# Performance work log

Measured on AMD Instinct MI355X. Metric: run time of the kernel, lower is better.

The kernel has to match this reference:

```python
import jax, jax.numpy as jnp
import numpy as np

MAX_DISP = 40  # search range -> D = 2*MAX_DISP+1 = 81 cost channels
STRIDE = 1


def setup_inputs() -> dict:
    key = jax.random.key(0)
    k1, k2 = jax.random.split(key)
    B, C, H, W = 4, 256, 128, 416
    left = jax.random.normal(k1, (B, C, H, W), dtype=jnp.float32)
    right = jax.random.normal(k2, (B, C, H, W), dtype=jnp.float32)
    return {"left": left, "right": right}


def reference(left, right):
    # mode='time', reduction='mean': per horizontal shift i, cost = mean_C(left * shift(right, i))
    B, C, H, W = left.shape
    rp = jnp.pad(right, ((0, 0), (0, 0), (0, 0), (MAX_DISP, MAX_DISP)))  # [B,C,H,W+2M]
    costs = []
    for i in range(-MAX_DISP, MAX_DISP + 1, STRIDE):  # fixed small unrolled loop over 81 shifts
        sl = jax.lax.dynamic_slice_in_dim(rp, i + MAX_DISP, W, axis=3)  # [B,C,H,W]
        costs.append(jnp.mean(left * sl, axis=1, keepdims=True))        # [B,1,H,W]
    return jnp.concatenate(costs, axis=1)  # [B, 81, H, W]
```

## Files before the change

### kernel.cpp

```cpp
#include <hip/hip_runtime.h>
#include <hip/hip_bf16.h>
#include <stdint.h>

typedef __bf16 bf16x8 __attribute__((ext_vector_type(8)));
typedef float f32x4 __attribute__((ext_vector_type(4)));

#define MAXD 40
#define ND   81
#define CSZ  256
#define HSZ  128
#define WSZ  416
#define HW   (HSZ * WSZ)

#define ALC  448
#define EL   0
#define ER   7168
#define OL   14336
#define ORR  21504
#define ESTR 420

union U8 { uint32_t u[4]; bf16x8 v; };

static __device__ __forceinline__ uint32_t pk2(float a, float b) {
    union { __bf16 h[2]; uint32_t u; } v;
    v.h[0] = (__bf16)a; v.h[1] = (__bf16)b;
    return v.u;
}

static __device__ __forceinline__ void gl16(const float* g, const float* l) {
    __builtin_amdgcn_global_load_lds(
        (const __attribute__((address_space(1))) void*)(uintptr_t)g,
        (__attribute__((address_space(3))) void*)(uint32_t)(uintptr_t)l,
        16, 0, 0);
}

static __device__ __forceinline__ void full_barrier() {
    asm volatile("s_waitcnt vmcnt(0) lgkmcnt(0)" ::: "memory");
    __builtin_amdgcn_s_barrier();
    __builtin_amdgcn_sched_barrier(0);
}

__global__ __launch_bounds__(1024)
void corr_mfma_kernel(const float* __restrict__ left,
                      const float* __restrict__ right,
                      float* __restrict__ out) {
    __shared__ float Sh[28672];

    const int t   = threadIdx.x;
    const int wv  = t >> 6;
    const int l   = t & 63;
    const int l15 = l & 15;
    const int l4  = l >> 4;
    const int b   = blockIdx.x >> 7;
    const int h   = blockIdx.x & 127;

    const size_t slab = ((size_t)b * CSZ) * HW + (size_t)h * WSZ;
    const float* gLw = left  + slab + (size_t)wv * HW + 4 * l;
    const float* gRw = right + slab + (size_t)wv * HW + 4 * l;
    const int shw = 8 * ((wv >> 2) & 3);
    const float* dEL = &Sh[EL  + wv * ALC + shw];
    const float* dER = &Sh[ER  + wv * ALC + shw];
    const float* dOL = &Sh[OL  + wv * ALC + shw];
    const float* dOR = &Sh[ORR + wv * ALC + shw];

    const int p0 = 2 * wv;
    const bool hasP1 = (wv < 15);
    int  cb[2]; bool okb[2];
    #pragma unroll
    for (int pi = 0; pi < 2; ++pi) {
        const int u = 16 * (p0 + pi) - MAXD + l15;
        okb[pi] = ((unsigned)u < (unsigned)WSZ);
        cb[pi]  = okb[pi] ? u : 0;
    }
    const int FB = 1800 * l4;

    f32x4 acc0[6], acc1[6];
    #pragma unroll
    for (int k = 0; k < 6; ++k) { acc0[k] = (f32x4)0.0f; acc1[k] = (f32x4)0.0f; }

    {
        gl16(gLw, dEL); gl16(gRw, dER);
        if (l < 40) { gl16(gLw + 256, dEL + 256); gl16(gRw + 256, dER + 256); }
    }
    full_barrier();

    for (int m = 0; m < 8; ++m) {
        {
            const size_t co = (size_t)(2 * m + 1) * 16 * HW;
            gl16(gLw + co, dOL); gl16(gRw + co, dOR);
            if (l < 40) { gl16(gLw + co + 256, dOL + 256); gl16(gRw + co + 256, dOR + 256); }
        }
        uint2 aLo[7], bLo[2];
        #pragma unroll
        for (int pi = 0; pi < 2; ++pi) {
            if (pi == 0 || hasP1) {
                float v0 = Sh[ER + FB +   0 + cb[pi]];
                float v1 = Sh[ER + FB + 448 + cb[pi]];
                float v2 = Sh[ER + FB + 896 + cb[pi]];
                float v3 = Sh[ER + FB + 1344 + cb[pi]];
                if (!okb[pi]) { v0 = v1 = v2 = v3 = 0.0f; }
                bLo[pi] = make_uint2(pk2(v0, v1), pk2(v2, v3));
            } else bLo[pi] = make_uint2(0u, 0u);
        }
        #pragma unroll
        for (int a = 0; a < 7; ++a) {
            const int r = p0 - 5 + a;
            if (r >= 0 && r <= 25) {
                const int col = 16 * r + l15;
                const float v0 = Sh[EL + FB +   0 + col];
                const float v1 = Sh[EL + FB + 448 + col];
                const float v2 = Sh[EL + FB + 896 + col];
                const float v3 = Sh[EL + FB + 1344 + col];
                aLo[a] = make_uint2(pk2(v0, v1), pk2(v2, v3));
            } else aLo[a] = make_uint2(0u, 0u);
        }
        full_barrier();

        if (m < 7) {
            const size_t co = (size_t)(2 * m + 2) * 16 * HW;
            gl16(gLw + co, dEL); gl16(gRw + co, dER);
            if (l < 40) { gl16(gLw + co + 256, dEL + 256); gl16(gRw + co + 256, dER + 256); }
        }
        bf16x8 bF[2];
        #pragma unroll
        for (int pi = 0; pi < 2; ++pi) {
            if (pi == 0 || hasP1) {
                float v0 = Sh[ORR + FB +   0 + cb[pi]];
                float v1 = Sh[ORR + FB + 448 + cb[pi]];
                float v2 = Sh[ORR + FB + 896 + cb[pi]];
                float v3 = Sh[ORR + FB + 1344 + cb[pi]];
                if (!okb[pi]) { v0 = v1 = v2 = v3 = 0.0f; }
                U8 x; x.u[0] = bLo[pi].x; x.u[1] = bLo[pi].y;
                x.u[2] = pk2(v0, v1); x.u[3] = pk2(v2, v3);
                bF[pi] = x.v;
            }
        }
        #pragma unroll
        for (int a = 0; a < 7; ++a) {
            const int r = p0 - 5 + a;
            if (r >= 0 && r <= 25) {
                const int col = 16 * r + l15;
                const float v0 = Sh[OL + FB +   0 + col];
                const float v1 = Sh[OL + FB + 448 + col];
                const float v2 = Sh[OL + FB + 896 + col];
                const float v3 = Sh[OL + FB + 1344 + col];
                U8 x; x.u[0] = aLo[a].x; x.u[1] = aLo[a].y;
                x.u[2] = pk2(v0, v1); x.u[3] = pk2(v2, v3);
                if (a < 6)
                    acc0[a] = __builtin_amdgcn_mfma_f32_16x16x32_bf16(x.v, bF[0], acc0[a], 0, 0, 0);
                if (hasP1 && a >= 1)
                    acc1[a - 1] = __builtin_amdgcn_mfma_f32_16x16x32_bf16(x.v, bF[1], acc1[a - 1], 0, 0, 0);
            }
        }
        full_barrier();
    }

    const float scale = 1.0f / 256.0f;
    float* outp = out + (size_t)b * ND * HW + (size_t)h * WSZ;

    #pragma unroll
    for (int gph = 0; gph < 2; ++gph) {
        const int d0 = gph * 41;
        const int dn = gph ? 40 : 41;

        #pragma unroll
        for (int pi = 0; pi < 2; ++pi) {
            if (pi == 0 || hasP1) {
                #pragma unroll
                for (int k = 0; k < 6; ++k) {
                    const int r = p0 - 5 + pi + k;
                    if (r >= 0 && r <= 25) {
                        const int j = 5 - k;
                        const f32x4 av = pi ? acc1[k] : acc0[k];
                        #pragma unroll
                        for (int rr = 0; rr < 4; ++rr) {
                            const int mm = 4 * l4 + rr;
                            const int d  = 16 * j + l15 - mm;
                            if ((unsigned)(d - d0) < (unsigned)dn)
                                Sh[(d - d0) * ESTR + 16 * r + mm] = av[rr] * scale;
                        }
                    }
                }
            }
        }
        full_barrier();

        #pragma unroll
        for (int i = 0; i < 5; ++i) {
            const int idx = i * 1024 + t;
            if (idx < dn * 104) {
                const int d = idx / 104;
                const int q = idx - 104 * d;
                *(f32x4*)(outp + (size_t)(d0 + d) * HW + 4 * q) = *(const f32x4*)&Sh[d * ESTR + 4 * q];
            }
        }
        if (gph == 0) full_barrier();
    }
}

extern "C" void kernel_launch(void* const* d_in, const int* in_sizes, int n_in,
                              void* d_out, int out_size, void* d_ws, size_t ws_size,
                              hipStream_t stream) {
    const float* left  = (const float*)d_in[0];
    const float* right = (const float*)d_in[1];
    float* out = (float*)d_out;
    (void)in_sizes; (void)n_in; (void)out_size; (void)d_ws; (void)ws_size;
    corr_mfma_kernel<<<dim3(4 * 128), dim3(1024), 0, stream>>>(left, right, out);
}
```

Before: 101.6 us.

## Triple-buffer LDS channel chunks with prefetch depth two and partial vmcnt waits

Replaces the even/odd double buffer with a three-slot LDS ring, so each 16-channel chunk is prefetched two steps ahead. Barriers wait with vmcnt(4) instead of draining all outstanding global loads, which lets the next chunk's loads stay in flight during compute. The padded row stride and swizzle offset are dropped to fit three buffers, which risks more LDS bank conflicts and grows shared memory to about 160KB.

New measurement: 105.7 us. +4.1%, slower.

```diff
diff --git a/kernel.cpp b/kernel.cpp
--- a/kernel.cpp
+++ b/kernel.cpp
@@ -12,12 +12,11 @@
 #define WSZ  416
 #define HW   (HSZ * WSZ)
 
-#define ALC  448
-#define EL   0
-#define ER   7168
-#define OL   14336
-#define ORR  21504
-#define ESTR 420
+#define ALC   420
+#define RHALF 6720
+#define BUFD  13440
+#define NCHK  16
+#define ESTR  420
 
 union U8 { uint32_t u[4]; bf16x8 v; };
 
@@ -34,17 +33,11 @@
         16, 0, 0);
 }
 
-static __device__ __forceinline__ void full_barrier() {
-    asm volatile("s_waitcnt vmcnt(0) lgkmcnt(0)" ::: "memory");
-    __builtin_amdgcn_s_barrier();
-    __builtin_amdgcn_sched_barrier(0);
-}
-
 __global__ __launch_bounds__(1024)
 void corr_mfma_kernel(const float* __restrict__ left,
                       const float* __restrict__ right,
                       float* __restrict__ out) {
-    __shared__ float Sh[28672];
+    __shared__ float Sh[3 * BUFD];
 
     const int t   = threadIdx.x;
     const int wv  = t >> 6;
@@ -55,104 +48,121 @@
     const int h   = blockIdx.x & 127;
 
     const size_t slab = ((size_t)b * CSZ) * HW + (size_t)h * WSZ;
-    const float* gLw = left  + slab + (size_t)wv * HW + 4 * l;
-    const float* gRw = right + slab + (size_t)wv * HW + 4 * l;
-    const int shw = 8 * ((wv >> 2) & 3);
-    const float* dEL = &Sh[EL  + wv * ALC + shw];
-    const float* dER = &Sh[ER  + wv * ALC + shw];
-    const float* dOL = &Sh[OL  + wv * ALC + shw];
-    const float* dOR = &Sh[ORR + wv * ALC + shw];
+    const float* Lw = left  + slab + (size_t)wv * HW + 4 * l;
+    const float* Rw = right + slab + (size_t)wv * HW + 4 * l;
 
     const int p0 = 2 * wv;
     const bool hasP1 = (wv < 15);
-    int  cb[2]; bool okb[2];
+    int cb[2]; bool okb[2];
     #pragma unroll
     for (int pi = 0; pi < 2; ++pi) {
         const int u = 16 * (p0 + pi) - MAXD + l15;
         okb[pi] = ((unsigned)u < (unsigned)WSZ);
         cb[pi]  = okb[pi] ? u : 0;
     }
-    const int FB = 1800 * l4;
+    const int FB = 1680 * l4;
 
     f32x4 acc0[6], acc1[6];
     #pragma unroll
     for (int k = 0; k < 6; ++k) { acc0[k] = (f32x4)0.0f; acc1[k] = (f32x4)0.0f; }
 
-    {
-        gl16(gLw, dEL); gl16(gRw, dER);
-        if (l < 40) { gl16(gLw + 256, dEL + 256); gl16(gRw + 256, dER + 256); }
-    }
-    full_barrier();
-
-    for (int m = 0; m < 8; ++m) {
-        {
-            const size_t co = (size_t)(2 * m + 1) * 16 * HW;
-            gl16(gLw + co, dOL); gl16(gRw + co, dOR);
-            if (l < 40) { gl16(gLw + co + 256, dOL + 256); gl16(gRw + co + 256, dOR + 256); }
-        }
-        uint2 aLo[7], bLo[2];
-        #pragma unroll
-        for (int pi = 0; pi < 2; ++pi) {
-            if (pi == 0 || hasP1) {
-                float v0 = Sh[ER + FB +   0 + cb[pi]];
-                float v1 = Sh[ER + FB + 448 + cb[pi]];
-                float v2 = Sh[ER + FB + 896 + cb[pi]];
-                float v3 = Sh[ER + FB + 1344 + cb[pi]];
-                if (!okb[pi]) { v0 = v1 = v2 = v3 = 0.0f; }
-                bLo[pi] = make_uint2(pk2(v0, v1), pk2(v2, v3));
-            } else bLo[pi] = make_uint2(0u, 0u);
-        }
-        #pragma unroll
-        for (int a = 0; a < 7; ++a) {
-            const int r = p0 - 5 + a;
-            if (r >= 0 && r <= 25) {
-                const int col = 16 * r + l15;
-                const float v0 = Sh[EL + FB +   0 + col];
-                const float v1 = Sh[EL + FB + 448 + col];
-                const float v2 = Sh[EL + FB + 896 + col];
-                const float v3 = Sh[EL + FB + 1344 + col];
-                aLo[a] = make_uint2(pk2(v0, v1), pk2(v2, v3));
-            } else aLo[a] = make_uint2(0u, 0u);
-        }
-        full_barrier();
-
-        if (m < 7) {
-            const size_t co = (size_t)(2 * m + 2) * 16 * HW;
-            gl16(gLw + co, dEL); gl16(gRw + co, dER);
-            if (l < 40) { gl16(gLw + co + 256, dEL + 256); gl16(gRw + co + 256, dER + 256); }
-        }
-        bf16x8 bF[2];
-        #pragma unroll
-        for (int pi = 0; pi < 2; ++pi) {
-            if (pi == 0 || hasP1) {
-                float v0 = Sh[ORR + FB +   0 + cb[pi]];
-                float v1 = Sh[ORR + FB + 448 + cb[pi]];
-                float v2 = Sh[ORR + FB + 896 + cb[pi]];
-                float v3 = Sh[ORR + FB + 1344 + cb[pi]];
-                if (!okb[pi]) { v0 = v1 = v2 = v3 = 0.0f; }
-                U8 x; x.u[0] = bLo[pi].x; x.u[1] = bLo[pi].y;
-                x.u[2] = pk2(v0, v1); x.u[3] = pk2(v2, v3);
-                bF[pi] = x.v;
-            }
-        }
-        #pragma unroll
-        for (int a = 0; a < 7; ++a) {
-            const int r = p0 - 5 + a;
-            if (r >= 0 && r <= 25) {
-                const int col = 16 * r + l15;
-                const float v0 = Sh[OL + FB +   0 + col];
-                const float v1 = Sh[OL + FB + 448 + col];
-                const float v2 = Sh[OL + FB + 896 + col];
-                const float v3 = Sh[OL + FB + 1344 + col];
-                U8 x; x.u[0] = aLo[a].x; x.u[1] = aLo[a].y;
-                x.u[2] = pk2(v0, v1); x.u[3] = pk2(v2, v3);
-                if (a < 6)
-                    acc0[a] = __builtin_amdgcn_mfma_f32_16x16x32_bf16(x.v, bF[0], acc0[a], 0, 0, 0);
-                if (hasP1 && a >= 1)
-                    acc1[a - 1] = __builtin_amdgcn_mfma_f32_16x16x32_bf16(x.v, bF[1], acc1[a - 1], 0, 0, 0);
-            }
-        }
-        full_barrier();
+    uint2 aLo[7], bLo[2];
+
+    #pragma unroll
+    for (int c0 = 0; c0 < 2; ++c0) {
+        const float* gL = Lw + (size_t)(16 * c0) * HW;
+        const float* gR = Rw + (size_t)(16 * c0) * HW;
+        const float* dL = &Sh[BUFD * c0 + wv * ALC];
+        const float* dR = &Sh[BUFD * c0 + RHALF + wv * ALC];
+        gl16(gL, dL); gl16(gR, dR);
+        if (l < 40) { gl16(gL + 256, dL + 256); gl16(gR + 256, dR + 256); }
+    }
+    asm volatile("s_waitcnt vmcnt(4) lgkmcnt(0)" ::: "memory");
+    __builtin_amdgcn_s_barrier();
+    __builtin_amdgcn_sched_barrier(0);
+
+    #pragma unroll
+    for (int ck = 0; ck < NCHK; ++ck) {
+        if (ck + 2 < NCHK) {
+            const int buf = BUFD * ((ck + 2) % 3);
+            const float* gL = Lw + (size_t)(16 * (ck + 2)) * HW;
+            const float* gR = Rw + (size_t)(16 * (ck + 2)) * HW;
+            const float* dL = &Sh[buf + wv * ALC];
+            const float* dR = &Sh[buf + RHALF + wv * ALC];
+            gl16(gL, dL); gl16(gR, dR);
+            if (l < 40) { gl16(gL + 256, dL + 256); gl16(gR + 256, dR + 256); }
+        }
+
+        const int cbuf = BUFD * (ck % 3);
+
+        if ((ck & 1) == 0) {
+            #pragma unroll
+            for (int pi = 0; pi < 2; ++pi) {
+                if (pi == 0 || hasP1) {
+                    float v0 = Sh[cbuf + RHALF + FB + 0 * ALC + cb[pi]];
+                    float v1 = Sh[cbuf + RHALF + FB + 1 * ALC + cb[pi]];
+                    float v2 = Sh[cbuf + RHALF + FB + 2 * ALC + cb[pi]];
+                    float v3 = Sh[cbuf + RHALF + FB + 3 * ALC + cb[pi]];
+                    if (!okb[pi]) { v0 = v1 = v2 = v3 = 0.0f; }
+                    bLo[pi] = make_uint2(pk2(v0, v1), pk2(v2, v3));
+                } else bLo[pi] = make_uint2(0u, 0u);
+            }
+            #pragma unroll
+            for (int a = 0; a < 7; ++a) {
+                const int r = p0 - 5 + a;
+                if (r >= 0 && r <= 25) {
+                    const int col = 16 * r + l15;
+                    const float v0 = Sh[cbuf + FB + 0 * ALC + col];
+                    const float v1 = Sh[cbuf + FB + 1 * ALC + col];
+                    const float v2 = Sh[cbuf + FB + 2 * ALC + col];
+                    const float v3 = Sh[cbuf + FB + 3 * ALC + col];
+                    aLo[a] = make_uint2(pk2(v0, v1), pk2(v2, v3));
+                } else aLo[a] = make_uint2(0u, 0u);
+            }
+        } else {
+            bf16x8 bF[2];
+            #pragma unroll
+            for (int pi = 0; pi < 2; ++pi) {
+                if (pi == 0 || hasP1) {
+                    float v0 = Sh[cbuf + RHALF + FB + 0 * ALC + cb[pi]];
+                    float v1 = Sh[cbuf + RHALF + FB + 1 * ALC + cb[pi]];
+                    float v2 = Sh[cbuf + RHALF + FB + 2 * ALC + cb[pi]];
+                    float v3 = Sh[cbuf + RHALF + FB + 3 * ALC + cb[pi]];
+                    if (!okb[pi]) { v0 = v1 = v2 = v3 = 0.0f; }
+                    U8 x; x.u[0] = bLo[pi].x; x.u[1] = bLo[pi].y;
+                    x.u[2] = pk2(v0, v1); x.u[3] = pk2(v2, v3);
+                    bF[pi] = x.v;
+                } else {
+                    U8 z; z.u[0] = z.u[1] = z.u[2] = z.u[3] = 0u;
+                    bF[pi] = z.v;
+                }
+            }
+            #pragma unroll
+            for (int a = 0; a < 7; ++a) {
+                const int r = p0 - 5 + a;
+                if (r >= 0 && r <= 25) {
+                    const int col = 16 * r + l15;
+                    const float v0 = Sh[cbuf + FB + 0 * ALC + col];
+                    const float v1 = Sh[cbuf + FB + 1 * ALC + col];
+                    const float v2 = Sh[cbuf + FB + 2 * ALC + col];
+                    const float v3 = Sh[cbuf + FB + 3 * ALC + col];
+                    U8 x; x.u[0] = aLo[a].x; x.u[1] = aLo[a].y;
+                    x.u[2] = pk2(v0, v1); x.u[3] = pk2(v2, v3);
+                    if (a < 6)
+                        acc0[a] = __builtin_amdgcn_mfma_f32_16x16x32_bf16(x.v, bF[0], acc0[a], 0, 0, 0);
+                    if (hasP1 && a >= 1)
+                        acc1[a - 1] = __builtin_amdgcn_mfma_f32_16x16x32_bf16(x.v, bF[1], acc1[a - 1], 0, 0, 0);
+                }
+            }
+        }
+
+        if (ck + 2 < NCHK) {
+            asm volatile("s_waitcnt vmcnt(4) lgkmcnt(0)" ::: "memory");
+        } else {
+            asm volatile("s_waitcnt vmcnt(0) lgkmcnt(0)" ::: "memory");
+        }
+        __builtin_amdgcn_s_barrier();
+        __builtin_amdgcn_sched_barrier(0);
     }
 
     const float scale = 1.0f / 256.0f;
@@ -183,7 +193,9 @@
                 }
             }
         }
-        full_barrier();
+        asm volatile("s_waitcnt lgkmcnt(0)" ::: "memory");
+        __builtin_amdgcn_s_barrier();
+        __builtin_amdgcn_sched_barrier(0);
 
         #pragma unroll
         for (int i = 0; i < 5; ++i) {
@@ -194,7 +206,11 @@
                 *(f32x4*)(outp + (size_t)(d0 + d) * HW + 4 * q) = *(const f32x4*)&Sh[d * ESTR + 4 * q];
             }
         }
-        if (gph == 0) full_barrier();
+        if (gph == 0) {
+            asm volatile("s_waitcnt lgkmcnt(0)" ::: "memory");
+            __builtin_amdgcn_s_barrier();
+            __builtin_amdgcn_sched_barrier(0);
+        }
     }
 }
 
```

## Process two rows per block, prefetch next row during epilogue, shrink LDS

Applied to the files above, without the earlier changes.

Each block now handles two consecutive image rows, halving the grid to 256 blocks. The first chunk of the second row is prefetched into LDS while the first row's last chunk is still being computed. The per-wave LDS stride drops from 448 to 420 floats with no bank-shift offset, and the output staging uses three 27-channel groups in the odd buffers with LDS-only barriers. The goal is to hide row startup latency and overlap output stores with the next row's loads. In exchange, 256 blocks is fewer than one per CU on a 256-CU part, and removing the bank shift may cause LDS bank conflicts.

Measured after the change: 169.2 us. +66.6%, slower.

```diff
diff --git a/kernel.cpp b/kernel.cpp
--- a/kernel.cpp
+++ b/kernel.cpp
@@ -12,11 +12,11 @@
 #define WSZ  416
 #define HW   (HSZ * WSZ)
 
-#define ALC  448
+#define ALC  420
 #define EL   0
-#define ER   7168
-#define OL   14336
-#define ORR  21504
+#define ER   6720
+#define OL   13440
+#define ORR  20160
 #define ESTR 420
 
 union U8 { uint32_t u[4]; bf16x8 v; };
@@ -40,161 +40,181 @@
     __builtin_amdgcn_sched_barrier(0);
 }
 
+static __device__ __forceinline__ void lds_barrier() {
+    asm volatile("s_waitcnt lgkmcnt(0)" ::: "memory");
+    __builtin_amdgcn_s_barrier();
+    __builtin_amdgcn_sched_barrier(0);
+}
+
 __global__ __launch_bounds__(1024)
 void corr_mfma_kernel(const float* __restrict__ left,
                       const float* __restrict__ right,
                       float* __restrict__ out) {
-    __shared__ float Sh[28672];
+    __shared__ float Sh[26880];
 
     const int t   = threadIdx.x;
     const int wv  = t >> 6;
     const int l   = t & 63;
     const int l15 = l & 15;
     const int l4  = l >> 4;
-    const int b   = blockIdx.x >> 7;
-    const int h   = blockIdx.x & 127;
-
-    const size_t slab = ((size_t)b * CSZ) * HW + (size_t)h * WSZ;
-    const float* gLw = left  + slab + (size_t)wv * HW + 4 * l;
-    const float* gRw = right + slab + (size_t)wv * HW + 4 * l;
-    const int shw = 8 * ((wv >> 2) & 3);
-    const float* dEL = &Sh[EL  + wv * ALC + shw];
-    const float* dER = &Sh[ER  + wv * ALC + shw];
-    const float* dOL = &Sh[OL  + wv * ALC + shw];
-    const float* dOR = &Sh[ORR + wv * ALC + shw];
+    const int b   = blockIdx.x >> 6;
+    const int hp  = blockIdx.x & 63;
 
     const int p0 = 2 * wv;
     const bool hasP1 = (wv < 15);
-    int  cb[2]; bool okb[2];
+    int cb[2]; bool okb[2];
     #pragma unroll
     for (int pi = 0; pi < 2; ++pi) {
         const int u = 16 * (p0 + pi) - MAXD + l15;
         okb[pi] = ((unsigned)u < (unsigned)WSZ);
         cb[pi]  = okb[pi] ? u : 0;
     }
-    const int FB = 1800 * l4;
+    const int FB = 1680 * l4;
+
+    const float* dEL = &Sh[EL  + wv * ALC];
+    const float* dER = &Sh[ER  + wv * ALC];
+    const float* dOL = &Sh[OL  + wv * ALC];
+    const float* dOR = &Sh[ORR + wv * ALC];
 
     f32x4 acc0[6], acc1[6];
     #pragma unroll
     for (int k = 0; k < 6; ++k) { acc0[k] = (f32x4)0.0f; acc1[k] = (f32x4)0.0f; }
 
-    {
-        gl16(gLw, dEL); gl16(gRw, dER);
-        if (l < 40) { gl16(gLw + 256, dEL + 256); gl16(gRw + 256, dER + 256); }
-    }
+    const size_t slab0 = ((size_t)b * CSZ) * HW + (size_t)(2 * hp) * WSZ;
+    const float* gLw = left  + slab0 + (size_t)wv * HW + 4 * l;
+    const float* gRw = right + slab0 + (size_t)wv * HW + 4 * l;
+
+    gl16(gLw, dEL); gl16(gRw, dER);
+    if (l < 40) { gl16(gLw + 256, dEL + 256); gl16(gRw + 256, dER + 256); }
     full_barrier();
 
-    for (int m = 0; m < 8; ++m) {
-        {
-            const size_t co = (size_t)(2 * m + 1) * 16 * HW;
-            gl16(gLw + co, dOL); gl16(gRw + co, dOR);
-            if (l < 40) { gl16(gLw + co + 256, dOL + 256); gl16(gRw + co + 256, dOR + 256); }
+    const float scale = 1.0f / 256.0f;
+
+    for (int s = 0; s < 2; ++s) {
+        const float* Ls = gLw + (size_t)s * WSZ;
+        const float* Rs = gRw + (size_t)s * WSZ;
+
+        for (int m = 0; m < 8; ++m) {
+            {
+                const size_t co = (size_t)(2 * m + 1) * 16 * HW;
+                gl16(Ls + co, dOL); gl16(Rs + co, dOR);
+                if (l < 40) { gl16(Ls + co + 256, dOL + 256); gl16(Rs + co + 256, dOR + 256); }
+            }
+            uint2 aLo[7], bLo[2];
+            #pragma unroll
+            for (int pi = 0; pi < 2; ++pi) {
+                if (pi == 0 || hasP1) {
+                    float v0 = Sh[ER + FB +    0 + cb[pi]];
+                    float v1 = Sh[ER + FB +  420 + cb[pi]];
+                    float v2 = Sh[ER + FB +  840 + cb[pi]];
+                    float v3 = Sh[ER + FB + 1260 + cb[pi]];
+                    if (!okb[pi]) { v0 = v1 = v2 = v3 = 0.0f; }
+                    bLo[pi] = make_uint2(pk2(v0, v1), pk2(v2, v3));
+                } else bLo[pi] = make_uint2(0u, 0u);
+            }
+            #pragma unroll
+            for (int a = 0; a < 7; ++a) {
+                const int r = p0 - 5 + a;
+                if (r >= 0 && r <= 25) {
+                    const int col = 16 * r + l15;
+                    const float v0 = Sh[EL + FB +    0 + col];
+                    const float v1 = Sh[EL + FB +  420 + col];
+                    const float v2 = Sh[EL + FB +  840 + col];
+                    const float v3 = Sh[EL + FB + 1260 + col];
+                    aLo[a] = make_uint2(pk2(v0, v1), pk2(v2, v3));
+                } else aLo[a] = make_uint2(0u, 0u);
+            }
+            full_barrier();
+
+            if (m < 7) {
+                const size_t co = (size_t)(2 * m + 2) * 16 * HW;
+                gl16(Ls + co, dEL); gl16(Rs + co, dER);
+                if (l < 40) { gl16(Ls + co + 256, dEL + 256); gl16(Rs + co + 256, dER + 256); }
+            } else if (s == 0) {
+                const float* Ln = gLw + WSZ;
+                const float* Rn = gRw + WSZ;
+                gl16(Ln, dEL); gl16(Rn, dER);
+                if (l < 40) { gl16(Ln + 256, dEL + 256); gl16(Rn + 256, dER + 256); }
+            }
+            bf16x8 bF[2];
+            #pragma unroll
+            for (int pi = 0; pi < 2; ++pi) {
+                if (pi == 0 || hasP1) {
+                    float v0 = Sh[ORR + FB +    0 + cb[pi]];
+                    float v1 = Sh[ORR + FB +  420 + cb[pi]];
+                    float v2 = Sh[ORR + FB +  840 + cb[pi]];
+                    float v3 = Sh[ORR + FB + 1260 + cb[pi]];
+                    if (!okb[pi]) { v0 = v1 = v2 = v3 = 0.0f; }
+                    U8 x; x.u[0] = bLo[pi].x; x.u[1] = bLo[pi].y;
+                    x.u[2] = pk2(v0, v1); x.u[3] = pk2(v2, v3);
+                    bF[pi] = x.v;
+                } else {
+                    U8 z; z.u[0] = z.u[1] = z.u[2] = z.u[3] = 0u;
+                    bF[pi] = z.v;
+                }
+            }
+            #pragma unroll
+            for (int a = 0; a < 7; ++a) {
+                const int r = p0 - 5 + a;
+                if (r >= 0 && r <= 25) {
+                    const int col = 16 * r + l15;
+                    const float v0 = Sh[OL + FB +    0 + col];
+                    const float v1 = Sh[OL + FB +  420 + col];
+                    const float v2 = Sh[OL + FB +  840 + col];
+                    const float v3 = Sh[OL + FB + 1260 + col];
+                    U8 x; x.u[0] = aLo[a].x; x.u[1] = aLo[a].y;
+                    x.u[2] = pk2(v0, v1); x.u[3] = pk2(v2, v3);
+                    if (a < 6)
+                        acc0[a] = __builtin_amdgcn_mfma_f32_16x16x32_bf16(x.v, bF[0], acc0[a], 0, 0, 0);
+                    if (hasP1 && a >= 1)
+                        acc1[a - 1] = __builtin_amdgcn_mfma_f32_16x16x32_bf16(x.v, bF[1], acc1[a - 1], 0, 0, 0);
+                }
+            }
+            full_barrier();
         }
-        uint2 aLo[7], bLo[2];
-        #pragma unroll
-        for (int pi = 0; pi < 2; ++pi) {
-            if (pi == 0 || hasP1) {
-                float v0 = Sh[ER + FB +   0 + cb[pi]];
-                float v1 = Sh[ER + FB + 448 + cb[pi]];
-                float v2 = Sh[ER + FB + 896 + cb[pi]];
-                float v3 = Sh[ER + FB + 1344 + cb[pi]];
-                if (!okb[pi]) { v0 = v1 = v2 = v3 = 0.0f; }
-                bLo[pi] = make_uint2(pk2(v0, v1), pk2(v2, v3));
-            } else bLo[pi] = make_uint2(0u, 0u);
-        }
-        #pragma unroll
-        for (int a = 0; a < 7; ++a) {
-            const int r = p0 - 5 + a;
-            if (r >= 0 && r <= 25) {
-                const int col = 16 * r + l15;
-                const float v0 = Sh[EL + FB +   0 + col];
-                const float v1 = Sh[EL + FB + 448 + col];
-                const float v2 = Sh[EL + FB + 896 + col];
-                const float v3 = Sh[EL + FB + 1344 + col];
-                aLo[a] = make_uint2(pk2(v0, v1), pk2(v2, v3));
-            } else aLo[a] = make_uint2(0u, 0u);
-        }
-        full_barrier();
-
-        if (m < 7) {
-            const size_t co = (size_t)(2 * m + 2) * 16 * HW;
-            gl16(gLw + co, dEL); gl16(gRw + co, dER);
-            if (l < 40) { gl16(gLw + co + 256, dEL + 256); gl16(gRw + co + 256, dER + 256); }
-        }
-        bf16x8 bF[2];
-        #pragma unroll
-        for (int pi = 0; pi < 2; ++pi) {
-            if (pi == 0 || hasP1) {
-                float v0 = Sh[ORR + FB +   0 + cb[pi]];
-                float v1 = Sh[ORR + FB + 448 + cb[pi]];
-                float v2 = Sh[ORR + FB + 896 + cb[pi]];
-                float v3 = Sh[ORR + FB + 1344 + cb[pi]];
-                if (!okb[pi]) { v0 = v1 = v2 = v3 = 0.0f; }
-                U8 x; x.u[0] = bLo[pi].x; x.u[1] = bLo[pi].y;
-                x.u[2] = pk2(v0, v1); x.u[3] = pk2(v2, v3);
-                bF[pi] = x.v;
-            }
-        }
-        #pragma unroll
-        for (int a = 0; a < 7; ++a) {
-            const int r = p0 - 5 + a;
-            if (r >= 0 && r <= 25) {
-                const int col = 16 * r + l15;
-                const float v0 = Sh[OL + FB +   0 + col];
-                const float v1 = Sh[OL + FB + 448 + col];
-                const float v2 = Sh[OL + FB + 896 + col];
-                const float v3 = Sh[OL + FB + 1344 + col];
-                U8 x; x.u[0] = aLo[a].x; x.u[1] = aLo[a].y;
-                x.u[2] = pk2(v0, v1); x.u[3] = pk2(v2, v3);
-                if (a < 6)
-                    acc0[a] = __builtin_amdgcn_mfma_f32_16x16x32_bf16(x.v, bF[0], acc0[a], 0, 0, 0);
-                if (hasP1 && a >= 1)
-                    acc1[a - 1] = __builtin_amdgcn_mfma_f32_16x16x32_bf16(x.v, bF[1], acc1[a - 1], 0, 0, 0);
-            }
-        }
-        full_barrier();
-    }
-
-    const float scale = 1.0f / 256.0f;
-    float* outp = out + (size_t)b * ND * HW + (size_t)h * WSZ;
-
-    #pragma unroll
-    for (int gph = 0; gph < 2; ++gph) {
-        const int d0 = gph * 41;
-        const int dn = gph ? 40 : 41;
-
-        #pragma unroll
-        for (int pi = 0; pi < 2; ++pi) {
-            if (pi == 0 || hasP1) {
-                #pragma unroll
-                for (int k = 0; k < 6; ++k) {
-                    const int r = p0 - 5 + pi + k;
-                    if (r >= 0 && r <= 25) {
-                        const int j = 5 - k;
-                        const f32x4 av = pi ? acc1[k] : acc0[k];
-                        #pragma unroll
-                        for (int rr = 0; rr < 4; ++rr) {
-                            const int mm = 4 * l4 + rr;
-                            const int d  = 16 * j + l15 - mm;
-                            if ((unsigned)(d - d0) < (unsigned)dn)
-                                Sh[(d - d0) * ESTR + 16 * r + mm] = av[rr] * scale;
+
+        float* outp = out + (size_t)b * ND * HW + (size_t)(2 * hp + s) * WSZ;
+        float* Shf = &Sh[OL];
+
+        for (int g = 0; g < 3; ++g) {
+            const int d0 = 27 * g;
+            #pragma unroll
+            for (int pi = 0; pi < 2; ++pi) {
+                if (pi == 0 || hasP1) {
+                    #pragma unroll
+                    for (int k = 0; k < 6; ++k) {
+                        const int r = p0 - 5 + pi + k;
+                        if (r >= 0 && r <= 25) {
+                            const int j = 5 - k;
+                            const f32x4 av = pi ? acc1[k] : acc0[k];
+                            #pragma unroll
+                            for (int rr = 0; rr < 4; ++rr) {
+                                const int mm = 4 * l4 + rr;
+                                const int d  = 16 * j + l15 - mm;
+                                if ((unsigned)(d - d0) < 27u)
+                                    Shf[(d - d0) * ESTR + 16 * r + mm] = av[rr] * scale;
+                            }
                         }
                     }
                 }
             }
+            lds_barrier();
+            #pragma unroll
+            for (int i = 0; i < 3; ++i) {
+                const int idx = i * 1024 + t;
+                if (idx < 27 * 104) {
+                    const int d = idx / 104;
+                    const int q = idx - 104 * d;
+                    *(f32x4*)(outp + (size_t)(d0 + d) * HW + 4 * q) = *(const f32x4*)&Shf[d * ESTR + 4 * q];
+                }
+            }
+            lds_barrier();
         }
-        full_barrier();
-
-        #pragma unroll
-        for (int i = 0; i < 5; ++i) {
-            const int idx = i * 1024 + t;
-            if (idx < dn * 104) {
-                const int d = idx / 104;
-                const int q = idx - 104 * d;
-                *(f32x4*)(outp + (size_t)(d0 + d) * HW + 4 * q) = *(const f32x4*)&Sh[d * ESTR + 4 * q];
-            }
+
+        if (s == 0) {
+            #pragma unroll
+            for (int k = 0; k < 6; ++k) { acc0[k] = (f32x4)0.0f; acc1[k] = (f32x4)0.0f; }
         }
-        if (gph == 0) full_barrier();
     }
 }
 
@@ -205,5 +225,5 @@
     const float* right = (const float*)d_in[1];
     float* out = (float*)d_out;
     (void)in_sizes; (void)n_in; (void)out_size; (void)d_ws; (void)ws_size;
-    corr_mfma_kernel<<<dim3(4 * 128), dim3(1024), 0, stream>>>(left, right, out);
-}
+    corr_mfma_kernel<<<dim3(256), dim3(1024), 0, stream>>>(left, right, out);
+}
```
